# Performance work log

Hardware: AMD Instinct MI355X
Metric: run time of the kernel (lower is better)

## Reference

```python
import jax, jax.numpy as jnp
import numpy as np

MAX_NORM = 1.0
B, V, C, VOCAB, E = 256, 50, 32, 100000, 128


def setup_inputs() -> dict:
    key = jax.random.key(0)
    k1, k2, k3 = jax.random.split(key, 3)
    W = jax.random.normal(k1, (VOCAB, E), dtype=jnp.float32)
    codes = jax.random.randint(k2, (B, V, C), 0, VOCAB, dtype=jnp.int64)
    n_visits = jax.random.randint(k3, (B,), 1, V + 1, dtype=jnp.int64)
    # ensure batch_max_visits == V (static output shape, matches min(max(len), max_visits))
    n_visits = n_visits.at[0].set(V)
    return {"W": W, "codes": codes, "n_visits": n_visits}


def reference(W, codes, n_visits):
    # Faithful to the torch module: expand_visits produces offsets [0,1,...,nv-1],
    # so EmbeddingBag('sum') bag i = emb(flat[i]) for i < nv-1, and the last bag
    # sums emb(flat[nv-1 : nv*C]). Result is top-padded to V rows per patient.
    b, v, c = codes.shape
    L = v * c
    flat = codes.reshape(b, L)                     # flattened codes per patient
    g = W[flat]                                    # [B, L, E] gathered rows
    # EmbeddingBag max_norm: renormalize looked-up rows whose norm exceeds MAX_NORM
    norms = jnp.linalg.norm(g, axis=-1, keepdims=True)
    g = g * jnp.minimum(1.0, MAX_NORM / jnp.maximum(norms, 1e-12))
    # prefix sums: cs0[:, j] = sum of g[:, :j]
    cs0 = jnp.concatenate([jnp.zeros((b, 1, g.shape[-1]), g.dtype),
                           jnp.cumsum(g, axis=1)], axis=1)  # [B, L+1, E]
    nv = n_visits.astype(jnp.int32)                # [B]
    end = (nv * c)[:, None, None]                  # sum over real flattened codes
    start = (nv - 1)[:, None, None]
    S = (jnp.take_along_axis(cs0, end, axis=1)
         - jnp.take_along_axis(cs0, start, axis=1))  # [B, 1, E] last-bag sum
    r = jnp.arange(v, dtype=jnp.int32)[None, :]    # output row index
    i = r - (v - nv[:, None])                      # bag index (negative => pad row)
    ei = jnp.take_along_axis(g, jnp.clip(i, 0, L - 1)[:, :, None], axis=1)  # [B, V, E]
    out = jnp.where((i >= 0)[:, :, None],
                    jnp.where((i < nv[:, None] - 1)[:, :, None], ei, S),
                    jnp.zeros_like(ei))
    return out
```

## Files before the change

kernel.cpp:

```cpp
#include <hip/hip_runtime.h>
#include <math.h>

#define B_     256
#define V_     50
#define C_     32
#define E_     128
#define VOCAB_ 100000
#define L_     (V_ * C_)
#define SPLIT  8

__global__ __launch_bounds__(1024) void scales_kernel(
    const float* __restrict__ W, float* __restrict__ scales)
{
    const int wave = threadIdx.x >> 6;
    const int lane = threadIdx.x & 63;
    const int r = blockIdx.x * 16 + wave;
    if (r >= VOCAB_) return;
    float2 v = ((const float2*)(W + (size_t)r * E_))[lane];
    float ss = v.x * v.x + v.y * v.y;
    #pragma unroll
    for (int off = 32; off > 0; off >>= 1) ss += __shfl_xor(ss, off, 64);
    if (lane == 0)
        scales[r] = fminf(1.0f, 1.0f / fmaxf(sqrtf(ss), 1e-12f));
}

__global__ __launch_bounds__(256) void singles_kernel(
    const float* __restrict__ W, const float* __restrict__ scales,
    const int* __restrict__ codes, const int* __restrict__ nvis,
    float* __restrict__ out)
{
    const int wg   = blockIdx.x * 4 + (threadIdx.x >> 6);
    const int lane = threadIdx.x & 63;
    const int b = wg / V_;
    const int i = wg % V_;
    if (b >= B_) return;
    const int nv = nvis[b];
    float* ob = out + (size_t)b * V_ * E_;

    if (i == V_ - 1) {
        ((float2*)(ob + (size_t)(V_ - 1) * E_))[lane] = make_float2(0.0f, 0.0f);
    } else if (i < nv - 1) {
        const int code = codes[b * L_ + i];
        const float sc = scales[code];
        float2 v = ((const float2*)(W + (size_t)code * E_))[lane];
        ((float2*)(ob + (size_t)(V_ - nv + i) * E_))[lane] =
            make_float2(v.x * sc, v.y * sc);
    } else {
        ((float2*)(ob + (size_t)(i - (nv - 1)) * E_))[lane] =
            make_float2(0.0f, 0.0f);
    }
}

__global__ __launch_bounds__(256) void bags_kernel(
    const float* __restrict__ W, const float* __restrict__ scales,
    const int* __restrict__ codes, const int* __restrict__ nvis,
    float* __restrict__ out)
{
    const int b    = blockIdx.x / SPLIT;
    const int s    = blockIdx.x % SPLIT;
    const int wave = threadIdx.x >> 6;
    const int lane = threadIdx.x & 63;

    const int nv  = nvis[b];
    const int j0  = nv - 1;
    const int j1  = nv * C_;
    const int chunk = (j1 - j0 + SPLIT - 1) / SPLIT;
    const int a0 = j0 + s * chunk;
    const int a1 = min(a0 + chunk, j1);
    const int* cf = codes + b * L_;

    float ax = 0.0f, ay = 0.0f;
    #pragma unroll 8
    for (int j = a0 + wave; j < a1; j += 4) {
        const int code = cf[j];
        const float sc = scales[code];
        float2 v = ((const float2*)(W + (size_t)code * E_))[lane];
        ax += v.x * sc;
        ay += v.y * sc;
    }

    __shared__ float sx[4][64], sy[4][64];
    sx[wave][lane] = ax;
    sy[wave][lane] = ay;
    __syncthreads();
    if (wave == 0) {
        const float fx = sx[0][lane] + sx[1][lane] + sx[2][lane] + sx[3][lane];
        const float fy = sy[0][lane] + sy[1][lane] + sy[2][lane] + sy[3][lane];
        float* dst = out + ((size_t)b * V_ + (V_ - 1)) * E_;
        atomicAdd(&dst[2 * lane],     fx);
        atomicAdd(&dst[2 * lane + 1], fy);
    }
}

extern "C" void kernel_launch(void* const* d_in, const int* in_sizes, int n_in,
                              void* d_out, int out_size, void* d_ws, size_t ws_size,
                              hipStream_t stream) {
    const float* W     = (const float*)d_in[0];
    const int*   codes = (const int*)d_in[1];
    const int*   nvis  = (const int*)d_in[2];
    float*       out   = (float*)d_out;
    float*       scales = (float*)d_ws;

    scales_kernel<<<(VOCAB_ + 15) / 16, 1024, 0, stream>>>(W, scales);
    singles_kernel<<<(B_ * V_ + 3) / 4, 256, 0, stream>>>(W, scales, codes, nvis, out);
    bags_kernel<<<B_ * SPLIT, 256, 0, stream>>>(W, scales, codes, nvis, out);
}
```

Baseline: 116.9 us.

## Use float4 half-wave row loads and per-wave contiguous code chunks in bags

```diff
diff --git a/kernel.cpp b/kernel.cpp
--- a/kernel.cpp
+++ b/kernel.cpp
@@ -8,19 +8,21 @@
 #define VOCAB_ 100000
 #define L_     (V_ * C_)
 #define SPLIT  8
+#define NWB    (SPLIT * 4)
 
 __global__ __launch_bounds__(1024) void scales_kernel(
     const float* __restrict__ W, float* __restrict__ scales)
 {
     const int wave = threadIdx.x >> 6;
     const int lane = threadIdx.x & 63;
-    const int r = blockIdx.x * 16 + wave;
-    if (r >= VOCAB_) return;
-    float2 v = ((const float2*)(W + (size_t)r * E_))[lane];
-    float ss = v.x * v.x + v.y * v.y;
+    const int half = lane >> 5;
+    const int hl   = lane & 31;
+    const int r = blockIdx.x * 32 + wave * 2 + half;
+    float4 v = ((const float4*)(W + (size_t)r * E_))[hl];
+    float ss = v.x * v.x + v.y * v.y + v.z * v.z + v.w * v.w;
     #pragma unroll
-    for (int off = 32; off > 0; off >>= 1) ss += __shfl_xor(ss, off, 64);
-    if (lane == 0)
+    for (int m = 1; m <= 16; m <<= 1) ss += __shfl_xor(ss, m, 64);
+    if (hl == 0)
         scales[r] = fminf(1.0f, 1.0f / fmaxf(sqrtf(ss), 1e-12f));
 }
 
@@ -29,25 +31,24 @@
     const int* __restrict__ codes, const int* __restrict__ nvis,
     float* __restrict__ out)
 {
-    const int wg   = blockIdx.x * 4 + (threadIdx.x >> 6);
-    const int lane = threadIdx.x & 63;
-    const int b = wg / V_;
-    const int i = wg % V_;
-    if (b >= B_) return;
+    const int hwid = (blockIdx.x * 256 + threadIdx.x) >> 5;
+    const int hl   = threadIdx.x & 31;
+    const int b = hwid / V_;
+    const int i = hwid % V_;
     const int nv = nvis[b];
     float* ob = out + (size_t)b * V_ * E_;
 
     if (i == V_ - 1) {
-        ((float2*)(ob + (size_t)(V_ - 1) * E_))[lane] = make_float2(0.0f, 0.0f);
+        ((float4*)(ob + (size_t)(V_ - 1) * E_))[hl] = make_float4(0.f, 0.f, 0.f, 0.f);
     } else if (i < nv - 1) {
         const int code = codes[b * L_ + i];
         const float sc = scales[code];
-        float2 v = ((const float2*)(W + (size_t)code * E_))[lane];
-        ((float2*)(ob + (size_t)(V_ - nv + i) * E_))[lane] =
-            make_float2(v.x * sc, v.y * sc);
+        float4 v = ((const float4*)(W + (size_t)code * E_))[hl];
+        ((float4*)(ob + (size_t)(V_ - nv + i) * E_))[hl] =
+            make_float4(v.x * sc, v.y * sc, v.z * sc, v.w * sc);
     } else {
-        ((float2*)(ob + (size_t)(i - (nv - 1)) * E_))[lane] =
-            make_float2(0.0f, 0.0f);
+        ((float4*)(ob + (size_t)(i - (nv - 1)) * E_))[hl] =
+            make_float4(0.f, 0.f, 0.f, 0.f);
     }
 }
 
@@ -60,48 +61,69 @@
     const int s    = blockIdx.x % SPLIT;
     const int wave = threadIdx.x >> 6;
     const int lane = threadIdx.x & 63;
+    const int half = lane >> 5;
+    const int hl   = lane & 31;
 
-    const int nv  = nvis[b];
-    const int j0  = nv - 1;
-    const int j1  = nv * C_;
-    const int chunk = (j1 - j0 + SPLIT - 1) / SPLIT;
-    const int a0 = j0 + s * chunk;
-    const int a1 = min(a0 + chunk, j1);
-    const int* cf = codes + b * L_;
+    const int nv    = nvis[b];
+    const int j0    = nv - 1;
+    const int j1    = nv * C_;
+    const int total = j1 - j0;
+    const int chunk = (total + NWB - 1) / NWB;
+    const int wid   = s * 4 + wave;
+    const int a0    = j0 + wid * chunk;
+    const int n     = min(a0 + chunk, j1) - a0;
+    const int* cf   = codes + b * L_;
 
-    float ax = 0.0f, ay = 0.0f;
-    #pragma unroll 8
-    for (int j = a0 + wave; j < a1; j += 4) {
-        const int code = cf[j];
-        const float sc = scales[code];
-        float2 v = ((const float2*)(W + (size_t)code * E_))[lane];
-        ax += v.x * sc;
-        ay += v.y * sc;
+    int   cl = 0;
+    float sl = 0.0f;
+    if (lane < n) {
+        cl = cf[a0 + lane];
+        sl = scales[cl];
     }
 
-    __shared__ float sx[4][64], sy[4][64];
-    sx[wave][lane] = ax;
-    sy[wave][lane] = ay;
+    float ax = 0.f, ay = 0.f, az = 0.f, aw = 0.f;
+    #pragma unroll 4
+    for (int t = 0; t < n; t += 2) {
+        const int   tt   = t + half;
+        const int   code = __shfl(cl, tt, 64);
+        const float sc   = __shfl(sl, tt, 64);
+        float4 v = ((const float4*)(W + (size_t)code * E_))[hl];
+        ax += v.x * sc; ay += v.y * sc; az += v.z * sc; aw += v.w * sc;
+    }
+
+    ax += __shfl_xor(ax, 32, 64);
+    ay += __shfl_xor(ay, 32, 64);
+    az += __shfl_xor(az, 32, 64);
+    aw += __shfl_xor(aw, 32, 64);
+
+    __shared__ float sx[4][32], sy[4][32], sz[4][32], sw[4][32];
+    if (half == 0) {
+        sx[wave][hl] = ax; sy[wave][hl] = ay; sz[wave][hl] = az; sw[wave][hl] = aw;
+    }
     __syncthreads();
-    if (wave == 0) {
-        const float fx = sx[0][lane] + sx[1][lane] + sx[2][lane] + sx[3][lane];
-        const float fy = sy[0][lane] + sy[1][lane] + sy[2][lane] + sy[3][lane];
-        float* dst = out + ((size_t)b * V_ + (V_ - 1)) * E_;
-        atomicAdd(&dst[2 * lane],     fx);
-        atomicAdd(&dst[2 * lane + 1], fy);
+    if (threadIdx.x < 32) {
+        const float fx = sx[0][hl] + sx[1][hl] + sx[2][hl] + sx[3][hl];
+        const float fy = sy[0][hl] + sy[1][hl] + sy[2][hl] + sy[3][hl];
+        const float fz = sz[0][hl] + sz[1][hl] + sz[2][hl] + sz[3][hl];
+        const float fw = sw[0][hl] + sw[1][hl] + sw[2][hl] + sw[3][hl];
+        float* dst = out + ((size_t)b * V_ + (V_ - 1)) * E_ + 4 * hl;
+        atomicAdd(&dst[0], fx);
+        atomicAdd(&dst[1], fy);
+        atomicAdd(&dst[2], fz);
+        atomicAdd(&dst[3], fw);
     }
 }
 
 extern "C" void kernel_launch(void* const* d_in, const int* in_sizes, int n_in,
                               void* d_out, int out_size, void* d_ws, size_t ws_size,
                               hipStream_t stream) {
-    const float* W     = (const float*)d_in[0];
-    const int*   codes = (const int*)d_in[1];
-    const int*   nvis  = (const int*)d_in[2];
-    float*       out   = (float*)d_out;
+    const float* W      = (const float*)d_in[0];
+    const int*   codes  = (const int*)d_in[1];
+    const int*   nvis   = (const int*)d_in[2];
+    float*       out    = (float*)d_out;
     float*       scales = (float*)d_ws;
 
-    scales_kernel<<<(VOCAB_ + 15) / 16, 1024, 0, stream>>>(W, scales);
-    singles_kernel<<<(B_ * V_ + 3) / 4, 256, 0, stream>>>(W, scales, codes, nvis, out);
-    bags_kernel<<<B_ * SPLIT, 256, 0, stream>>>(W, scales, codes, nvis, out);
+    scales_kernel <<<VOCAB_ / 32, 1024, 0, stream>>>(W, scales);
+    singles_kernel<<<B_ * V_ / 8, 256, 0, stream>>>(W, scales, codes, nvis, out);
+    bags_kernel   <<<B_ * SPLIT, 256, 0, stream>>>(W, scales, codes, nvis, out);
 }
```

After: 109.0 us. -6.7%, faster.
